# Performance work log

Measured on AMD Instinct MI355X. Metric: run time of the kernel, lower is better.

## Reference

```python
import jax, jax.numpy as jnp
import numpy as np

ACT_BITS = 8  # config.activation_bits
HIDDEN = 2048
INTERMEDIATE = 4096  # hidden * mlp_ratio (2.0), power of 2
EPS = 1e-5


def fwht(x):
    """Normalized fast Walsh-Hadamard transform along last axis (n = power of 2)."""
    shape = x.shape
    n = shape[-1]
    x = x.reshape(-1, n)
    h = 1
    while h < n:  # log2(n) fixed iterations, not a data-dim loop
        x = x.reshape(-1, n // (2 * h), 2, h)
        a, b = x[:, :, 0, :], x[:, :, 1, :]
        x = jnp.stack((a + b, a - b), axis=2).reshape(-1, n)
        h *= 2
    return (x * (1.0 / np.sqrt(n))).reshape(shape)


def _ste(x, q):
    # straight-through estimator: forward uses q, backward passes grad to x
    return x + jax.lax.stop_gradient(q - x)


def act_quant(x, bits):
    """Per-token absmax quantization to `bits` bits (BitNet a8 style), dequantized."""
    qb = float(2 ** (bits - 1) - 1)
    scale = qb / jnp.clip(jnp.max(jnp.abs(x), axis=-1, keepdims=True), EPS, None)
    q = jnp.clip(jnp.round(x * scale), -qb, qb) / scale
    return _ste(x, q)


def weight_quant(w):
    """Ternary absmean weight quantization (BitNet b1.58), dequantized."""
    scale = jnp.clip(jnp.mean(jnp.abs(w)), EPS, None)
    q = jnp.clip(jnp.round(w / scale), -1.0, 1.0) * scale
    return _ste(w, q)


def hbitlinear(x, w, bits):
    # H-BitLinear: Hadamard-rotate activations, quantize acts + weights, GEMM
    xq = act_quant(fwht(x), bits)
    wq = weight_quant(w)
    return jnp.einsum('bsd,fd->bsf', xq, wq)


def setup_inputs() -> dict:
    key = jax.random.key(0)
    k1, k2, k3 = jax.random.split(key, 3)
    hidden_states = jax.random.normal(k1, (4, 4096, HIDDEN), dtype=jnp.float32)
    w_up = jax.random.normal(k2, (INTERMEDIATE, HIDDEN), dtype=jnp.float32) * 0.02
    w_down = jax.random.normal(k3, (HIDDEN, INTERMEDIATE), dtype=jnp.float32) * 0.02
    return {"hidden_states": hidden_states, "w_up": w_up, "w_down": w_down}


def reference(hidden_states, w_up, w_down):
    h = hbitlinear(hidden_states, w_up, ACT_BITS)      # (B, S, intermediate)
    h = jnp.square(jax.nn.relu(h))                     # squared ReLU
    # dropout p=0.0 -> identity in eval/reference
    return hbitlinear(h, w_down, ACT_BITS)             # (B, S, hidden)
```

## Files before the change

### kernel.cpp

```cpp
#include <hip/hip_runtime.h>
#include <hip/hip_fp16.h>
#include <cstdint>
#include <cstddef>

#define HIDDEN 2048
#define INTER  4096
#define EPSQ   1e-5f

typedef int v4i __attribute__((ext_vector_type(4)));

__device__ __forceinline__ void async_ld16(const void* g, void* l) {
  __builtin_amdgcn_global_load_lds((const __attribute__((address_space(1))) void*)g,
                                   (__attribute__((address_space(3))) void*)l, 16, 0, 0);
}

__global__ void absmean_kernel(const float* __restrict__ w, size_t n4, double* __restrict__ out) {
  double s = 0.0;
  const float4* w4 = (const float4*)w;
  for (size_t i = blockIdx.x * (size_t)blockDim.x + threadIdx.x; i < n4;
       i += (size_t)gridDim.x * blockDim.x) {
    float4 v = w4[i];
    s += (double)fabsf(v.x) + (double)fabsf(v.y) + (double)fabsf(v.z) + (double)fabsf(v.w);
  }
  #pragma unroll
  for (int o = 32; o; o >>= 1) s += __shfl_down(s, o);
  __shared__ double red[4];
  if ((threadIdx.x & 63) == 0) red[threadIdx.x >> 6] = s;
  __syncthreads();
  if (threadIdx.x == 0) atomicAdd(out, red[0] + red[1] + red[2] + red[3]);
}

__global__ void quantw_kernel(const float* __restrict__ w, size_t n4,
                              const double* __restrict__ sum, double invcnt,
                              int8_t* __restrict__ q) {
  const float scale = (float)fmax(sum[0] * invcnt, (double)EPSQ);
  const float4* w4 = (const float4*)w;
  char4* q4 = (char4*)q;
  for (size_t i = blockIdx.x * (size_t)blockDim.x + threadIdx.x; i < n4;
       i += (size_t)gridDim.x * blockDim.x) {
    float4 v = w4[i];
    char4 c;
    c.x = (signed char)fmaxf(-1.f, fminf(1.f, rintf(v.x / scale)));
    c.y = (signed char)fmaxf(-1.f, fminf(1.f, rintf(v.y / scale)));
    c.z = (signed char)fmaxf(-1.f, fminf(1.f, rintf(v.z / scale)));
    c.w = (signed char)fmaxf(-1.f, fminf(1.f, rintf(v.w / scale)));
    q4[i] = c;
  }
}

template <int LOGN, bool HALF_IN>
__global__ void __launch_bounds__(256) fwht_quant_kernel(const void* __restrict__ Xv,
                                                         int8_t* __restrict__ Q,
                                                         float* __restrict__ invs) {
  constexpr int N = 1 << LOGN;
  constexpr int E = N / 64;
  const int lane = threadIdx.x & 63;
  const size_t t = (size_t)blockIdx.x * 4 + (threadIdx.x >> 6);

  float r[E];
  if constexpr (HALF_IN) {
    const int4* xp = (const int4*)((const __half*)Xv + t * (size_t)N + lane * E);
    #pragma unroll
    for (int u = 0; u < E / 8; ++u) {
      alignas(16) __half hb[8];
      *(int4*)hb = xp[u];
      #pragma unroll
      for (int j = 0; j < 8; ++j) r[u * 8 + j] = __half2float(hb[j]);
    }
  } else {
    const float4* xp = (const float4*)((const float*)Xv + t * (size_t)N + lane * E);
    #pragma unroll
    for (int u = 0; u < E / 4; ++u) {
      float4 v = xp[u];
      r[u * 4 + 0] = v.x; r[u * 4 + 1] = v.y; r[u * 4 + 2] = v.z; r[u * 4 + 3] = v.w;
    }
  }

  #pragma unroll
  for (int m = 1; m < E; m <<= 1) {
    #pragma unroll
    for (int e = 0; e < E; ++e) {
      if (!(e & m)) {
        float a = r[e], b = r[e | m];
        r[e] = a + b;
        r[e | m] = a - b;
      }
    }
  }
  #pragma unroll
  for (int m = 1; m < 64; m <<= 1) {
    const float sgn = (lane & m) ? -1.f : 1.f;
    #pragma unroll
    for (int e = 0; e < E; ++e) {
      float w = __shfl_xor(r[e], m, 64);
      r[e] = fmaf(r[e], sgn, w);
    }
  }

  float mx = 0.f;
  #pragma unroll
  for (int e = 0; e < E; ++e) mx = fmaxf(mx, fabsf(r[e]));
  #pragma unroll
  for (int m = 1; m < 64; m <<= 1) mx = fmaxf(mx, __shfl_xor(mx, m, 64));

  constexpr float c = (LOGN == 11) ? 0.022097086912079608f : 0.015625f;
  mx = fmaxf(mx * c, EPSQ);
  const float sc = 127.0f * c / mx;
  if (lane == 0) invs[t] = mx * (1.0f / 127.0f);

  alignas(16) int8_t qv[E];
  #pragma unroll
  for (int e = 0; e < E; ++e) {
    float q = rintf(r[e] * sc);
    q = fmaxf(-127.f, fminf(127.f, q));
    qv[e] = (int8_t)q;
  }
  int8_t* qp = Q + t * (size_t)N + lane * E;
  #pragma unroll
  for (int u = 0; u < E / 16; ++u) ((int4*)qp)[u] = ((const int4*)qv)[u];
}

template <bool RELU2, typename TOUT>
__global__ void gemm_i8_kernel(const int8_t* __restrict__ A, const int8_t* __restrict__ B,
                               TOUT* __restrict__ C, const float* __restrict__ invs,
                               const double* __restrict__ wsum, double invcnt,
                               int N, int K) {
  __shared__ int8_t As[128 * 64];
  __shared__ int8_t Bs[128 * 64];
  const int tid = threadIdx.x;
  const int lane = tid & 63, wave = tid >> 6;
  const int wr = wave >> 1, wc = wave & 1;
  const int m0 = blockIdx.y * 128, n0 = blockIdx.x * 128;

  v4i acc[4][4] = {};

  const int row = tid >> 2;
  const int colb = (tid & 3) * 16;
  const int8_t* gA0 = A + (size_t)(m0 + row) * K + colb;
  const int8_t* gA1 = A + (size_t)(m0 + row + 64) * K + colb;
  const int8_t* gB0 = B + (size_t)(n0 + row) * K + colb;
  const int8_t* gB1 = B + (size_t)(n0 + row + 64) * K + colb;
  int8_t* lA0 = As + tid * 16;
  int8_t* lA1 = As + 4096 + tid * 16;
  int8_t* lB0 = Bs + tid * 16;
  int8_t* lB1 = Bs + 4096 + tid * 16;

  const int afrag = (wr * 64 + (lane & 15)) * 64 + (lane >> 4) * 16;
  const int bfrag = (wc * 64 + (lane & 15)) * 64 + (lane >> 4) * 16;

  for (int k0 = 0; k0 < K; k0 += 64) {
    async_ld16(gA0 + k0, lA0);
    async_ld16(gA1 + k0, lA1);
    async_ld16(gB0 + k0, lB0);
    async_ld16(gB1 + k0, lB1);
    __syncthreads();
    v4i a[4], b[4];
    #pragma unroll
    for (int mt = 0; mt < 4; ++mt) a[mt] = *(const v4i*)(As + afrag + mt * 1024);
    #pragma unroll
    for (int nt = 0; nt < 4; ++nt) b[nt] = *(const v4i*)(Bs + bfrag + nt * 1024);
    #pragma unroll
    for (int mt = 0; mt < 4; ++mt)
      #pragma unroll
      for (int nt = 0; nt < 4; ++nt)
        acc[mt][nt] = __builtin_amdgcn_mfma_i32_16x16x64_i8(a[mt], b[nt], acc[mt][nt], 0, 0, 0);
    __syncthreads();
  }

  const float wscale = (float)fmax(wsum[0] * invcnt, (double)EPSQ);
  #pragma unroll
  for (int mt = 0; mt < 4; ++mt) {
    const int trow = m0 + wr * 64 + mt * 16 + (lane >> 4) * 4;
    float fr[4];
    #pragma unroll
    for (int r = 0; r < 4; ++r) fr[r] = wscale * invs[trow + r];
    const int col = n0 + wc * 64 + (lane & 15);
    #pragma unroll
    for (int nt = 0; nt < 4; ++nt) {
      #pragma unroll
      for (int r = 0; r < 4; ++r) {
        float v = (float)acc[mt][nt][r] * fr[r];
        if (RELU2) v = v > 0.f ? v * v : 0.f;
        if constexpr (sizeof(TOUT) == 2)
          C[(size_t)(trow + r) * N + (col + nt * 16)] = __float2half(v);
        else
          C[(size_t)(trow + r) * N + (col + nt * 16)] = v;
      }
    }
  }
}

extern "C" void kernel_launch(void* const* d_in, const int* in_sizes, int n_in,
                              void* d_out, int out_size, void* d_ws, size_t ws_size,
                              hipStream_t stream) {
  const float* x      = (const float*)d_in[0];
  const float* w_up   = (const float*)d_in[1];
  const float* w_down = (const float*)d_in[2];
  float* out = (float*)d_out;

  const int T = in_sizes[0] / HIDDEN;
  const size_t WN = (size_t)INTER * HIDDEN;

  char* ws = (char*)d_ws;
  double* sums   = (double*)ws;
  float* invs1   = (float*)(ws + 256);
  float* invs2   = (float*)(ws + 256 + 65536);
  int8_t* wq_up  = (int8_t*)(ws + 131328);
  int8_t* wq_dn  = wq_up + WN;
  int8_t* a8_1   = wq_dn + WN;
  int8_t* a8_2   = a8_1 + (size_t)T * HIDDEN;
  __half* h      = (__half*)(a8_2 + (size_t)T * INTER);

  const double invcnt = 1.0 / (double)WN;

  hipMemsetAsync(sums, 0, 256, stream);
  absmean_kernel<<<1024, 256, 0, stream>>>(w_up, WN / 4, sums + 0);
  absmean_kernel<<<1024, 256, 0, stream>>>(w_down, WN / 4, sums + 1);
  quantw_kernel<<<2048, 256, 0, stream>>>(w_up, WN / 4, sums + 0, invcnt, wq_up);
  quantw_kernel<<<2048, 256, 0, stream>>>(w_down, WN / 4, sums + 1, invcnt, wq_dn);

  fwht_quant_kernel<11, false><<<T / 4, 256, 0, stream>>>(x, a8_1, invs1);
  gemm_i8_kernel<true, __half><<<dim3(INTER / 128, T / 128), 256, 0, stream>>>(
      a8_1, wq_up, h, invs1, sums + 0, invcnt, INTER, HIDDEN);
  fwht_quant_kernel<12, true><<<T / 4, 256, 0, stream>>>(h, a8_2, invs2);
  gemm_i8_kernel<false, float><<<dim3(HIDDEN / 128, T / 128), 256, 0, stream>>>(
      a8_2, wq_dn, out, invs2, sums + 1, invcnt, HIDDEN, INTER);
}
```

Before: 690.1 us.

## Rewrite int8 GEMM as 256x256 double-buffered 8-phase pipelined kernel

Replaces the 128x128 single-buffered int8 MFMA GEMM with a 256x256-tile, 512-thread kernel using K=128 stages, double-buffered LDS, XOR-swizzled LDS layout and an 8-phase schedule that interleaves async global->LDS loads with MFMA work. It also remaps workgroup IDs across 8 groups for cache locality and raises MFMA priority with s_setprio. The aim is to hide global-load latency, cut LDS bank conflicts and raise arithmetic intensity. In exchange it uses 128KB of LDS and many accumulator registers, which limits occupancy, and the hand-tuned waitcnt/barrier ordering is fragile.

New measurement: 669.5 us. 1.03x faster.

```diff
diff --git a/kernel.cpp b/kernel.cpp
--- a/kernel.cpp
+++ b/kernel.cpp
@@ -13,6 +13,10 @@
   __builtin_amdgcn_global_load_lds((const __attribute__((address_space(1))) void*)g,
                                    (__attribute__((address_space(3))) void*)l, 16, 0, 0);
 }
+
+#define BAR()   __builtin_amdgcn_s_barrier()
+#define LGKM0() asm volatile("s_waitcnt lgkmcnt(0)" ::: "memory")
+#define VMC(n)  asm volatile("s_waitcnt vmcnt(" #n ")" ::: "memory")
 
 __global__ void absmean_kernel(const float* __restrict__ w, size_t n4, double* __restrict__ out) {
   double s = 0.0;
@@ -121,70 +125,148 @@
 }
 
 template <bool RELU2, typename TOUT>
-__global__ void gemm_i8_kernel(const int8_t* __restrict__ A, const int8_t* __restrict__ B,
-                               TOUT* __restrict__ C, const float* __restrict__ invs,
-                               const double* __restrict__ wsum, double invcnt,
-                               int N, int K) {
-  __shared__ int8_t As[128 * 64];
-  __shared__ int8_t Bs[128 * 64];
-  const int tid = threadIdx.x;
-  const int lane = tid & 63, wave = tid >> 6;
-  const int wr = wave >> 1, wc = wave & 1;
-  const int m0 = blockIdx.y * 128, n0 = blockIdx.x * 128;
-
-  v4i acc[4][4] = {};
-
-  const int row = tid >> 2;
-  const int colb = (tid & 3) * 16;
-  const int8_t* gA0 = A + (size_t)(m0 + row) * K + colb;
-  const int8_t* gA1 = A + (size_t)(m0 + row + 64) * K + colb;
-  const int8_t* gB0 = B + (size_t)(n0 + row) * K + colb;
-  const int8_t* gB1 = B + (size_t)(n0 + row + 64) * K + colb;
-  int8_t* lA0 = As + tid * 16;
-  int8_t* lA1 = As + 4096 + tid * 16;
-  int8_t* lB0 = Bs + tid * 16;
-  int8_t* lB1 = Bs + 4096 + tid * 16;
-
-  const int afrag = (wr * 64 + (lane & 15)) * 64 + (lane >> 4) * 16;
-  const int bfrag = (wc * 64 + (lane & 15)) * 64 + (lane >> 4) * 16;
-
-  for (int k0 = 0; k0 < K; k0 += 64) {
-    async_ld16(gA0 + k0, lA0);
-    async_ld16(gA1 + k0, lA1);
-    async_ld16(gB0 + k0, lB0);
-    async_ld16(gB1 + k0, lB1);
-    __syncthreads();
-    v4i a[4], b[4];
-    #pragma unroll
-    for (int mt = 0; mt < 4; ++mt) a[mt] = *(const v4i*)(As + afrag + mt * 1024);
-    #pragma unroll
-    for (int nt = 0; nt < 4; ++nt) b[nt] = *(const v4i*)(Bs + bfrag + nt * 1024);
+__global__ __launch_bounds__(512, 2)
+void gemm_i8_8ph(const int8_t* __restrict__ A, const int8_t* __restrict__ B,
+                 TOUT* __restrict__ C, const float* __restrict__ invs,
+                 const double* __restrict__ wsum, double invcnt,
+                 int N, int K) {
+  __shared__ int8_t As[2 * 2 * 128 * 128];
+  __shared__ int8_t Bs[2 * 2 * 128 * 128];
+
+  const int GX = N >> 8;
+  const int nwg = gridDim.x;
+  int wg = blockIdx.x;
+  wg = (wg & 7) * (nwg >> 3) + (wg >> 3);
+  const int bx = wg % GX;
+  const int by = wg / GX;
+  const int m0 = by * 256, n0 = bx * 256;
+
+  const int t = threadIdx.x;
+  const int lane = t & 63;
+  const int wave = t >> 6;
+  const int wr = wave >> 2;
+  const int wc = wave & 3;
+
+  const int row0 = t >> 3;
+  const int colsw = ((t & 7) * 16) ^ ((row0 & 7) << 4);
+  const int8_t* gA0 = A + (size_t)(m0 + row0) * K + colsw;
+  const int8_t* gA1 = gA0 + (size_t)128 * K;
+  const int8_t* gB0 = B + (size_t)(n0 + row0) * K + colsw;
+  const int8_t* gB1 = gB0 + (size_t)128 * K;
+  const size_t rstep = (size_t)64 * K;
+
+  auto SA = [&](int bf, int hf, int kt) {
+    const int8_t* g = (hf ? gA1 : gA0) + (size_t)kt * 128;
+    int8_t* l = As + bf * 32768 + hf * 16384 + t * 16;
+    async_ld16(g, l);
+    async_ld16(g + rstep, l + 8192);
+  };
+  auto SB = [&](int bf, int hf, int kt) {
+    const int8_t* g = (hf ? gB1 : gB0) + (size_t)kt * 128;
+    int8_t* l = Bs + bf * 32768 + hf * 16384 + t * 16;
+    async_ld16(g, l);
+    async_ld16(g + rstep, l + 8192);
+  };
+
+  const int csw0 = ((lane >> 4) * 16) ^ ((lane & 7) << 4);
+  const int csw1 = (64 + (lane >> 4) * 16) ^ ((lane & 7) << 4);
+  const int8_t* pA0 = As + wr * 16384 + (lane & 15) * 128;
+  const int8_t* pB0 = Bs + (wc >> 1) * 16384 + ((wc & 1) * 64 + (lane & 15)) * 128;
+
+  v4i acc[8][4] = {};
+  v4i a[4][2], b[4][2];
+
+  auto RDA = [&](int bf, int m4) {
+    const int8_t* p = pA0 + bf * 32768 + m4 * 8192;
+    #pragma unroll
+    for (int mt = 0; mt < 4; ++mt) {
+      a[mt][0] = *(const v4i*)(p + mt * 2048 + csw0);
+      a[mt][1] = *(const v4i*)(p + mt * 2048 + csw1);
+    }
+  };
+  auto RDB = [&](int bf, int n2) {
+    const int8_t* p = pB0 + bf * 32768 + n2 * 4096;
+    #pragma unroll
+    for (int nt = 0; nt < 2; ++nt) {
+      b[n2 * 2 + nt][0] = *(const v4i*)(p + nt * 2048 + csw0);
+      b[n2 * 2 + nt][1] = *(const v4i*)(p + nt * 2048 + csw1);
+    }
+  };
+  auto MM = [&](int m4, int n2) {
+    __builtin_amdgcn_s_setprio(1);
     #pragma unroll
     for (int mt = 0; mt < 4; ++mt)
       #pragma unroll
-      for (int nt = 0; nt < 4; ++nt)
-        acc[mt][nt] = __builtin_amdgcn_mfma_i32_16x16x64_i8(a[mt], b[nt], acc[mt][nt], 0, 0, 0);
-    __syncthreads();
+      for (int nt = 0; nt < 2; ++nt) {
+        v4i* c = &acc[m4 * 4 + mt][n2 * 2 + nt];
+        *c = __builtin_amdgcn_mfma_i32_16x16x64_i8(a[mt][0], b[n2 * 2 + nt][0], *c, 0, 0, 0);
+        *c = __builtin_amdgcn_mfma_i32_16x16x64_i8(a[mt][1], b[n2 * 2 + nt][1], *c, 0, 0, 0);
+      }
+    __builtin_amdgcn_s_setprio(0);
+  };
+
+  const int NIT = K >> 8;
+
+  SA(0, 0, 0); SA(0, 1, 0); SB(0, 0, 0); SB(0, 1, 0);
+  SA(1, 0, 1);
+  VMC(2);
+  BAR();
+
+  for (int it = 0; it < NIT; ++it) {
+    const int kt1 = 2 * it + 1, kt2 = 2 * it + 2, kt3 = 2 * it + 3;
+    const bool more = it < NIT - 1;
+
+    RDA(0, 0); RDB(0, 0);
+    SA(1, 1, kt1);
+    BAR(); LGKM0(); MM(0, 0); BAR();
+
+    RDB(0, 1);
+    SB(1, 0, kt1);
+    BAR(); LGKM0(); MM(0, 1); BAR();
+
+    RDA(0, 1);
+    SB(1, 1, kt1);
+    BAR(); LGKM0(); MM(1, 0); BAR();
+
+    if (more) { SA(0, 0, kt2); VMC(2); } else { VMC(0); }
+    BAR(); MM(1, 1); BAR();
+
+    RDA(1, 0); RDB(1, 0);
+    if (more) SA(0, 1, kt2);
+    BAR(); LGKM0(); MM(0, 0); BAR();
+
+    RDB(1, 1);
+    if (more) SB(0, 0, kt2);
+    BAR(); LGKM0(); MM(0, 1); BAR();
+
+    RDA(1, 1);
+    if (more) SB(0, 1, kt2);
+    BAR(); LGKM0(); MM(1, 0); BAR();
+
+    if (more) { SA(1, 0, kt3); VMC(2); }
+    BAR(); MM(1, 1); BAR();
   }
 
   const float wscale = (float)fmax(wsum[0] * invcnt, (double)EPSQ);
-  #pragma unroll
-  for (int mt = 0; mt < 4; ++mt) {
-    const int trow = m0 + wr * 64 + mt * 16 + (lane >> 4) * 4;
+  const int crow_base = m0 + wr * 128 + (lane >> 4) * 4;
+  const int ccol_base = n0 + wc * 64 + (lane & 15);
+  #pragma unroll
+  for (int mt = 0; mt < 8; ++mt) {
+    const int trow = crow_base + mt * 16;
     float fr[4];
     #pragma unroll
     for (int r = 0; r < 4; ++r) fr[r] = wscale * invs[trow + r];
-    const int col = n0 + wc * 64 + (lane & 15);
     #pragma unroll
     for (int nt = 0; nt < 4; ++nt) {
+      const int col = ccol_base + nt * 16;
       #pragma unroll
       for (int r = 0; r < 4; ++r) {
         float v = (float)acc[mt][nt][r] * fr[r];
         if (RELU2) v = v > 0.f ? v * v : 0.f;
         if constexpr (sizeof(TOUT) == 2)
-          C[(size_t)(trow + r) * N + (col + nt * 16)] = __float2half(v);
+          C[(size_t)(trow + r) * N + col] = __float2half(v);
         else
-          C[(size_t)(trow + r) * N + (col + nt * 16)] = v;
+          C[(size_t)(trow + r) * N + col] = v;
       }
     }
   }
@@ -220,9 +302,9 @@
   quantw_kernel<<<2048, 256, 0, stream>>>(w_down, WN / 4, sums + 1, invcnt, wq_dn);
 
   fwht_quant_kernel<11, false><<<T / 4, 256, 0, stream>>>(x, a8_1, invs1);
-  gemm_i8_kernel<true, __half><<<dim3(INTER / 128, T / 128), 256, 0, stream>>>(
+  gemm_i8_8ph<true, __half><<<(T / 256) * (INTER / 256), 512, 0, stream>>>(
       a8_1, wq_up, h, invs1, sums + 0, invcnt, INTER, HIDDEN);
   fwht_quant_kernel<12, true><<<T / 4, 256, 0, stream>>>(h, a8_2, invs2);
-  gemm_i8_kernel<false, float><<<dim3(HIDDEN / 128, T / 128), 256, 0, stream>>>(
+  gemm_i8_8ph<false, float><<<(T / 256) * (HIDDEN / 256), 512, 0, stream>>>(
       a8_2, wq_dn, out, invs2, sums + 1, invcnt, HIDDEN, INTER);
 }
```

## Rewrite int8 GEMM with 256x256 tiles, triple-buffered async loads, swizzled LDS

Applied to the files above, without the earlier changes.

Replaces the 128x128 single-buffered int8 GEMM with a 256x256-tile, 512-thread kernel. It uses a three-stage LDS ring filled by async global-to-LDS loads, with explicit vmcnt waits and barriers so the next tiles load while MFMAs run. It also adds an XOR swizzle on LDS chunks to cut bank conflicts, remaps workgroup IDs for locality, and raises MFMA priority with setprio. The cost is 96KB of LDS and more accumulator registers per block, which may limit occupancy.

After: 679.3 us. About the same (-1.6%).

```diff
diff --git a/kernel.cpp b/kernel.cpp
--- a/kernel.cpp
+++ b/kernel.cpp
@@ -13,6 +13,9 @@
   __builtin_amdgcn_global_load_lds((const __attribute__((address_space(1))) void*)g,
                                    (__attribute__((address_space(3))) void*)l, 16, 0, 0);
 }
+
+#define BAR()   __builtin_amdgcn_s_barrier()
+#define VMC(n)  asm volatile("s_waitcnt vmcnt(" #n ")" ::: "memory")
 
 __global__ void absmean_kernel(const float* __restrict__ w, size_t n4, double* __restrict__ out) {
   double s = 0.0;
@@ -121,70 +124,123 @@
 }
 
 template <bool RELU2, typename TOUT>
-__global__ void gemm_i8_kernel(const int8_t* __restrict__ A, const int8_t* __restrict__ B,
-                               TOUT* __restrict__ C, const float* __restrict__ invs,
-                               const double* __restrict__ wsum, double invcnt,
-                               int N, int K) {
-  __shared__ int8_t As[128 * 64];
-  __shared__ int8_t Bs[128 * 64];
-  const int tid = threadIdx.x;
-  const int lane = tid & 63, wave = tid >> 6;
-  const int wr = wave >> 1, wc = wave & 1;
-  const int m0 = blockIdx.y * 128, n0 = blockIdx.x * 128;
-
-  v4i acc[4][4] = {};
-
-  const int row = tid >> 2;
-  const int colb = (tid & 3) * 16;
-  const int8_t* gA0 = A + (size_t)(m0 + row) * K + colb;
-  const int8_t* gA1 = A + (size_t)(m0 + row + 64) * K + colb;
-  const int8_t* gB0 = B + (size_t)(n0 + row) * K + colb;
-  const int8_t* gB1 = B + (size_t)(n0 + row + 64) * K + colb;
-  int8_t* lA0 = As + tid * 16;
-  int8_t* lA1 = As + 4096 + tid * 16;
-  int8_t* lB0 = Bs + tid * 16;
-  int8_t* lB1 = Bs + 4096 + tid * 16;
-
-  const int afrag = (wr * 64 + (lane & 15)) * 64 + (lane >> 4) * 16;
-  const int bfrag = (wc * 64 + (lane & 15)) * 64 + (lane >> 4) * 16;
-
-  for (int k0 = 0; k0 < K; k0 += 64) {
-    async_ld16(gA0 + k0, lA0);
-    async_ld16(gA1 + k0, lA1);
-    async_ld16(gB0 + k0, lB0);
-    async_ld16(gB1 + k0, lB1);
-    __syncthreads();
-    v4i a[4], b[4];
-    #pragma unroll
-    for (int mt = 0; mt < 4; ++mt) a[mt] = *(const v4i*)(As + afrag + mt * 1024);
-    #pragma unroll
-    for (int nt = 0; nt < 4; ++nt) b[nt] = *(const v4i*)(Bs + bfrag + nt * 1024);
+__global__ __launch_bounds__(512, 2)
+void gemm_i8_3buf(const int8_t* __restrict__ A, const int8_t* __restrict__ B,
+                  TOUT* __restrict__ C, const float* __restrict__ invs,
+                  const double* __restrict__ wsum, double invcnt,
+                  int N, int K) {
+  __shared__ int8_t As[3 * 16384];
+  __shared__ int8_t Bs[3 * 16384];
+
+  const int GX = N >> 8;
+  const int nwg = gridDim.x;
+  int wg = blockIdx.x;
+  wg = (wg & 7) * (nwg >> 3) + (wg >> 3);
+  const int bx = wg % GX;
+  const int by = wg / GX;
+  const int m0 = by * 256, n0 = bx * 256;
+
+  const int t = threadIdx.x;
+  const int lane = t & 63;
+  const int wave = t >> 6;
+  const int wr = wave >> 2;
+  const int wc = wave & 3;
+
+  const int srow = t >> 2;
+  const int scol = (((t & 3) ^ ((t >> 3) & 3)) << 4);
+  const int8_t* gA = A + (size_t)(m0 + srow) * K + scol;
+  const int8_t* gB = B + (size_t)(n0 + srow) * K + scol;
+  const size_t rstep = (size_t)128 * K;
+  int8_t* lA = As + t * 16;
+  int8_t* lB = Bs + t * 16;
+
+  auto SA = [&](int buf, int kt) {
+    const int8_t* g = gA + (size_t)kt * 64;
+    async_ld16(g, lA + buf * 16384);
+    async_ld16(g + rstep, lA + buf * 16384 + 8192);
+  };
+  auto SB = [&](int buf, int kt) {
+    const int8_t* g = gB + (size_t)kt * 64;
+    async_ld16(g, lB + buf * 16384);
+    async_ld16(g + rstep, lB + buf * 16384 + 8192);
+  };
+
+  const int chunk_l = ((lane >> 4) ^ ((lane >> 1) & 3)) << 4;
+  const int8_t* pA = As + (wr * 128 + (lane & 15)) * 64 + chunk_l;
+  const int8_t* pB = Bs + (wc * 64 + (lane & 15)) * 64 + chunk_l;
+
+  v4i acc[8][4] = {};
+  v4i a[4], b[4];
+
+  auto RDA = [&](int buf, int m4) {
+    const int8_t* p = pA + buf * 16384 + m4 * 4096;
+    #pragma unroll
+    for (int mt = 0; mt < 4; ++mt) a[mt] = *(const v4i*)(p + mt * 1024);
+  };
+  auto RDB = [&](int buf) {
+    const int8_t* p = pB + buf * 16384;
+    #pragma unroll
+    for (int nt = 0; nt < 4; ++nt) b[nt] = *(const v4i*)(p + nt * 1024);
+  };
+  auto MM = [&](int m4) {
+    __builtin_amdgcn_s_setprio(1);
     #pragma unroll
     for (int mt = 0; mt < 4; ++mt)
       #pragma unroll
       for (int nt = 0; nt < 4; ++nt)
-        acc[mt][nt] = __builtin_amdgcn_mfma_i32_16x16x64_i8(a[mt], b[nt], acc[mt][nt], 0, 0, 0);
-    __syncthreads();
+        acc[m4 * 4 + mt][nt] =
+            __builtin_amdgcn_mfma_i32_16x16x64_i8(a[mt], b[nt], acc[m4 * 4 + mt][nt], 0, 0, 0);
+    __builtin_amdgcn_s_setprio(0);
+  };
+
+  const int NT = K >> 6;
+
+  SA(0, 0); SB(0, 0);
+  SA(1, 1); SB(1, 1);
+  VMC(4);
+  BAR();
+
+  int bk = 0, bs = 2;
+  for (int k = 0; k < NT; ++k) {
+    const bool st = (k + 2) < NT;
+
+    RDA(bk, 0); RDB(bk);
+    if (st) SA(bs, k + 2);
+    BAR(); MM(0); BAR();
+
+    RDA(bk, 1);
+    if (st) {
+      SB(bs, k + 2);
+      VMC(4);
+    } else if (k + 1 < NT) {
+      VMC(0);
+    }
+    BAR(); MM(1); BAR();
+
+    bk = (bk == 2) ? 0 : bk + 1;
+    bs = (bs == 2) ? 0 : bs + 1;
   }
 
   const float wscale = (float)fmax(wsum[0] * invcnt, (double)EPSQ);
-  #pragma unroll
-  for (int mt = 0; mt < 4; ++mt) {
-    const int trow = m0 + wr * 64 + mt * 16 + (lane >> 4) * 4;
+  const int crow_base = m0 + wr * 128 + (lane >> 4) * 4;
+  const int ccol_base = n0 + wc * 64 + (lane & 15);
+  #pragma unroll
+  for (int mt = 0; mt < 8; ++mt) {
+    const int trow = crow_base + (mt >> 2) * 64 + (mt & 3) * 16;
     float fr[4];
     #pragma unroll
     for (int r = 0; r < 4; ++r) fr[r] = wscale * invs[trow + r];
-    const int col = n0 + wc * 64 + (lane & 15);
     #pragma unroll
     for (int nt = 0; nt < 4; ++nt) {
+      const int col = ccol_base + nt * 16;
       #pragma unroll
       for (int r = 0; r < 4; ++r) {
         float v = (float)acc[mt][nt][r] * fr[r];
         if (RELU2) v = v > 0.f ? v * v : 0.f;
         if constexpr (sizeof(TOUT) == 2)
-          C[(size_t)(trow + r) * N + (col + nt * 16)] = __float2half(v);
+          C[(size_t)(trow + r) * N + col] = __float2half(v);
         else
-          C[(size_t)(trow + r) * N + (col + nt * 16)] = v;
+          C[(size_t)(trow + r) * N + col] = v;
       }
     }
   }
@@ -220,9 +276,9 @@
   quantw_kernel<<<2048, 256, 0, stream>>>(w_down, WN / 4, sums + 1, invcnt, wq_dn);
 
   fwht_quant_kernel<11, false><<<T / 4, 256, 0, stream>>>(x, a8_1, invs1);
-  gemm_i8_kernel<true, __half><<<dim3(INTER / 128, T / 128), 256, 0, stream>>>(
+  gemm_i8_3buf<true, __half><<<(T / 256) * (INTER / 256), 512, 0, stream>>>(
       a8_1, wq_up, h, invs1, sums + 0, invcnt, INTER, HIDDEN);
   fwht_quant_kernel<12, true><<<T / 4, 256, 0, stream>>>(h, a8_2, invs2);
-  gemm_i8_kernel<false, float><<<dim3(HIDDEN / 128, T / 128), 256, 0, stream>>>(
+  gemm_i8_3buf<false, float><<<(T / 256) * (HIDDEN / 256), 512, 0, stream>>>(
       a8_2, wq_dn, out, invs2, sums + 1, invcnt, HIDDEN, INTER);
 }
```
